# Kernel tuning notes

Measured on AMD Instinct MI355X. Metric: run time of the kernel, lower is better.

Reference implementation:

```python
import jax, jax.numpy as jnp
from jax import lax
import numpy as np

T, B = 64, 32          # timesteps, n_envs
C_IN, HW = 4, 64
H_LSTM = 256
FEAT = 64 * 4 * 4      # conv output flattened (1024)
FC = 512


def _conv(x, w, b, stride):
    # x: [N,C,H,W], w: [O,I,kh,kw] (torch OIHW), VALID padding like nn.Conv2d default
    y = lax.conv_general_dilated(x, w, (stride, stride), 'VALID',
                                 dimension_numbers=('NCHW', 'OIHW', 'NCHW'))
    return y + b[None, :, None, None]


def setup_inputs() -> dict:
    key = jax.random.key(0)
    ks = jax.random.split(key, 16)
    s = lambda *sh: sh
    d = {
        'x': jax.random.uniform(ks[0], (T * B, C_IN, HW, HW), jnp.float32) * 255.0,
        'done': jax.random.randint(ks[1], (T * B,), 0, 2, jnp.int32),
        'conv1_w': jax.random.normal(ks[2], (32, C_IN, 8, 8), jnp.float32) * 0.05,
        'conv1_b': jnp.zeros((32,), jnp.float32),
        'conv2_w': jax.random.normal(ks[3], (64, 32, 4, 4), jnp.float32) * 0.05,
        'conv2_b': jnp.zeros((64,), jnp.float32),
        'conv3_w': jax.random.normal(ks[4], (64, 64, 3, 3), jnp.float32) * 0.05,
        'conv3_b': jnp.zeros((64,), jnp.float32),
        'fc_w': jax.random.normal(ks[5], (FC, FEAT), jnp.float32) * 0.02,
        'fc_b': jnp.zeros((FC,), jnp.float32),
        'w_ih': jax.random.normal(ks[6], (4 * H_LSTM, FC), jnp.float32) * 0.03,
        'w_hh': jax.random.normal(ks[7], (4 * H_LSTM, H_LSTM), jnp.float32) * 0.03,
        'b_ih': jnp.zeros((4 * H_LSTM,), jnp.float32),
        'b_hh': jnp.zeros((4 * H_LSTM,), jnp.float32),
        'h0': jnp.zeros((1, B, H_LSTM), jnp.float32),
        'c0': jnp.zeros((1, B, H_LSTM), jnp.float32),
    }
    return d


def reference(x, done, conv1_w, conv1_b, conv2_w, conv2_b, conv3_w, conv3_b,
              fc_w, fc_b, w_ih, w_hh, b_ih, b_hh, h0, c0):
    # CNN encoder on x/255
    z = x / 255.0
    z = jax.nn.relu(_conv(z, conv1_w, conv1_b, 4))   # [TB,32,15,15]
    z = jax.nn.relu(_conv(z, conv2_w, conv2_b, 2))   # [TB,64,6,6]
    z = jax.nn.relu(_conv(z, conv3_w, conv3_b, 1))   # [TB,64,4,4]
    z = z.reshape(z.shape[0], -1)                    # [TB,1024]
    feats = jax.nn.relu(z @ fc_w.T + fc_b)           # [TB,512]

    n_envs = h0.shape[1]
    feats = feats.reshape(-1, n_envs, feats.shape[1])        # [T,B,512]
    mask = (1.0 - done.astype(feats.dtype)).reshape(-1, n_envs)  # [T,B]

    H = h0.shape[-1]

    def step(carry, inp):
        h, c = carry                    # [B,H] each
        f_t, m_t = inp                  # [B,512], [B]
        m = m_t[:, None]
        h = h * m
        c = c * m
        gates = f_t @ w_ih.T + b_ih + h @ w_hh.T + b_hh   # [B,4H]
        i, f, g, o = jnp.split(gates, 4, axis=-1)         # torch order: i,f,g,o
        c = jax.nn.sigmoid(f) * c + jax.nn.sigmoid(i) * jnp.tanh(g)
        h = jax.nn.sigmoid(o) * jnp.tanh(c)
        return (h, c), h

    (_, _), hs = lax.scan(step, (h0[0], c0[0]), (feats, mask))  # hs: [T,B,H]
    return hs.reshape(-1, H)   # [T*B, H]
```

## Files before the change

### kernel.cpp

```cpp
#include <hip/hip_runtime.h>
#include <math.h>


#define NIMG 2048

typedef _Float16 half2_t __attribute__((ext_vector_type(2)));
typedef __fp16 fp16x2_t __attribute__((ext_vector_type(2)));

__device__ inline unsigned short f2h_bits(float f) {
    union { _Float16 h; unsigned short u; } x;
    x.h = (_Float16)f;
    return x.u;
}

__device__ inline unsigned pack2_rne(float a, float b) {
    return (unsigned)f2h_bits(a) | ((unsigned)f2h_bits(b) << 16);
}

__device__ inline unsigned pack2_fast(float a, float b) {
#if __has_builtin(__builtin_amdgcn_cvt_pkrtz)
    union { fp16x2_t h; unsigned u; } x;
    x.h = __builtin_amdgcn_cvt_pkrtz(a, b);
    return x.u;
#else
    return pack2_rne(a, b);
#endif
}

__device__ inline float dot2(unsigned hu, unsigned wu, float acc) {
    union { unsigned u; half2_t h; } a, b;
    a.u = hu; b.u = wu;
#if __has_builtin(__builtin_amdgcn_fdot2)
    return __builtin_amdgcn_fdot2(a.h, b.h, acc, false);
#else
    return acc + (float)a.h.x * (float)b.h.x + (float)a.h.y * (float)b.h.y;
#endif
}

__device__ inline float fast_tanh(float x) {
    return 1.0f - 2.0f / (__expf(2.0f * x) + 1.0f);
}

__global__ void transpose_kernel(const float* __restrict__ in, float* __restrict__ out,
                                 int R, int C) {
    int idx = blockIdx.x * 256 + threadIdx.x;
    if (idx < R * C) {
        int r = idx / C, c = idx - r * C;
        out[c * R + r] = in[idx];
    }
}

__global__ void pack_whh_pairs_kernel(const float* __restrict__ whh,
                                      unsigned* __restrict__ wp) {
    int idx = blockIdx.x * 256 + threadIdx.x;
    if (idx >= 131072) return;
    int d4 = idx >> 12;
    int rem = idx & 4095;
    int row = rem >> 2;
    int j = idx & 3;
    int k0 = d4 * 8 + j * 2;
    const float* src = whh + (size_t)row * 256 + k0;
    wp[idx] = pack2_rne(src[0], src[1]);
}

__global__ void pack_w1_kernel(const float* __restrict__ w1, unsigned* __restrict__ w1p) {
    int idx = blockIdx.x * 256 + threadIdx.x;
    if (idx >= 4096) return;
    int oc = idx >> 7, rem = idx & 127;
    int ic = rem >> 5, ky = (rem >> 2) & 7, kxp = rem & 3;
    const float* src = w1 + (((size_t)oc * 4 + ic) * 8 + ky) * 8 + kxp * 2;
    w1p[idx] = pack2_rne(src[0], src[1]);
}

__global__ void pack_w2_kernel(const float* __restrict__ w2, unsigned* __restrict__ w2p) {
    int idx = blockIdx.x * 256 + threadIdx.x;
    if (idx >= 16384) return;
    int p = idx >> 6, oc = idx & 63;
    int ic = p >> 3, ky = (p >> 1) & 3, kxp = p & 1;
    const float* src = w2 + (size_t)oc * 512 + ic * 16 + ky * 4 + kxp * 2;
    w2p[idx] = pack2_rne(src[0], src[1]);
}

__global__ __launch_bounds__(1024) void conv1_kernel(const float* __restrict__ x,
                                                     const unsigned* __restrict__ w1p,
                                                     const float* __restrict__ b,
                                                     unsigned short* __restrict__ z1) {
    __shared__ unsigned short xs[4 * 64 * 64];
    int n = blockIdx.x;
    int tid = threadIdx.x;
    const float* xp = x + (size_t)n * 16384;
    const float inv = 1.0f / 255.0f;
    for (int i = tid * 4; i < 16384; i += 4096) {
        float4 v = *(const float4*)(xp + i);
        uint2 q;
        q.x = pack2_fast(v.x * inv, v.y * inv);
        q.y = pack2_fast(v.z * inv, v.w * inv);
        *(uint2*)&xs[i] = q;
    }
    __syncthreads();
    int lane = tid & 63, wave = tid >> 6;
    int gg = __builtin_amdgcn_readfirstlane(wave & 3);
    int pos = (wave >> 2) * 64 + lane;
    if (pos < 225) {
        int oy = pos / 15, ox = pos - oy * 15;
        float acc[8];
        const float* bp = b + gg * 8;
#pragma unroll
        for (int u = 0; u < 8; ++u) acc[u] = bp[u];
        for (int ic = 0; ic < 4; ++ic) {
#pragma unroll
            for (int ky = 0; ky < 8; ++ky) {
                const unsigned short* row = &xs[(ic * 64 + oy * 4 + ky) * 64 + ox * 4];
                uint2 qa = *(const uint2*)row;
                uint2 qb = *(const uint2*)(row + 4);
                const unsigned* wp = w1p + ((((gg * 8) * 4 + ic) * 8 + ky) * 4);
#pragma unroll
                for (int u = 0; u < 8; ++u) {
                    const unsigned* wu = wp + u * 128;
                    acc[u] = dot2(qa.x, wu[0], acc[u]);
                    acc[u] = dot2(qa.y, wu[1], acc[u]);
                    acc[u] = dot2(qb.x, wu[2], acc[u]);
                    acc[u] = dot2(qb.y, wu[3], acc[u]);
                }
            }
        }
        unsigned short* op = z1 + (size_t)n * 7680 + (gg * 8) * 240 + oy * 16 + ox;
#pragma unroll
        for (int u = 0; u < 8; ++u) op[u * 240] = f2h_bits(fmaxf(acc[u], 0.0f));
    }
}

__global__ __launch_bounds__(768) void conv2_kernel(const unsigned short* __restrict__ z1,
                                                    const unsigned* __restrict__ w2p,
                                                    const float* __restrict__ bias,
                                                    float* __restrict__ out) {
    __shared__ unsigned short xs[2][32 * 15 * 16];
    int tid = threadIdx.x;
    int n0 = blockIdx.x * 2;
#pragma unroll
    for (int img = 0; img < 2; ++img) {
        const unsigned* src = (const unsigned*)(z1 + (size_t)(n0 + img) * 7680);
        unsigned* dst = (unsigned*)xs[img];
        for (int i = tid; i < 3840; i += 768) dst[i] = src[i];
    }
    __syncthreads();
    int lane = tid & 63, wave = tid >> 6;
    int img = wave / 6;
    int oy = wave - img * 6;
    int n = n0 + img;
    float bv = bias[lane];
    float* op = out + (size_t)n * 2304 + lane * 36;
    float acc[6];
#pragma unroll
    for (int u = 0; u < 6; ++u) acc[u] = bv;
    for (int ic = 0; ic < 32; ++ic) {
#pragma unroll
        for (int ky = 0; ky < 4; ++ky) {
            const unsigned short* row = &xs[img][(ic * 15 + oy * 2 + ky) * 16];
            uint4 pa = *(const uint4*)row;
            uint4 pb = *(const uint4*)(row + 8);
            unsigned p[8] = {pa.x, pa.y, pa.z, pa.w, pb.x, pb.y, pb.z, pb.w};
            const unsigned* wpp = w2p + ((ic * 4 + ky) * 2) * 64 + lane;
            unsigned wa = wpp[0];
            unsigned wb = wpp[64];
#pragma unroll
            for (int u = 0; u < 6; ++u) {
                acc[u] = dot2(p[u], wa, acc[u]);
                acc[u] = dot2(p[u + 1], wb, acc[u]);
            }
        }
    }
#pragma unroll
    for (int u = 0; u < 6; ++u) op[oy * 6 + u] = fmaxf(acc[u], 0.0f);
}

__global__ __launch_bounds__(512) void conv3_kernel(const float* __restrict__ x,
                                                    const float* __restrict__ wt,
                                                    const float* __restrict__ bias,
                                                    float* __restrict__ out) {
    __shared__ float xs[4][64 * 6 * 8];
    int tid = threadIdx.x;
    int n0 = blockIdx.x * 4;
    for (int img = 0; img < 4; ++img) {
        const float* src = x + (size_t)(n0 + img) * 2304;
        for (int s = tid; s < 2304; s += 512) {
            int ic = s / 36;
            int rem = s - ic * 36;
            int r = rem / 6;
            int c = rem - r * 6;
            xs[img][(ic * 6 + r) * 8 + c] = src[s];
        }
    }
    __syncthreads();
    int lane = tid & 63, wave = tid >> 6;
    int img = wave >> 1;
    int half = wave & 1;
    int n = n0 + img;
    float bv = bias[lane];
    float* op = out + (size_t)n * 1024 + lane * 16;
    for (int q = 0; q < 2; ++q) {
        int oy = half * 2 + q;
        float acc[4];
#pragma unroll
        for (int u = 0; u < 4; ++u) acc[u] = bv;
        for (int ic = 0; ic < 64; ++ic) {
#pragma unroll
            for (int ky = 0; ky < 3; ++ky) {
                const float* xrow = &xs[img][(ic * 6 + oy + ky) * 8];
                float xr[8];
                *(float4*)&xr[0] = *(const float4*)&xrow[0];
                *(float4*)&xr[4] = *(const float4*)&xrow[4];
                const float* wp = wt + ((ic * 3 + ky) * 3) * 64 + lane;
#pragma unroll
                for (int kx = 0; kx < 3; ++kx) {
                    float wv = wp[kx * 64];
#pragma unroll
                    for (int u = 0; u < 4; ++u) acc[u] += xr[u + kx] * wv;
                }
            }
        }
#pragma unroll
        for (int u = 0; u < 4; ++u) op[oy * 4 + u] = fmaxf(acc[u], 0.0f);
    }
}

__global__ __launch_bounds__(256) void gemm_bt(const float* __restrict__ A,
                                               const float* __restrict__ B,
                                               const float* __restrict__ bias,
                                               const float* __restrict__ bias2,
                                               float* __restrict__ C,
                                               int M, int N, int K, int relu) {
    __shared__ float As[16][68];
    __shared__ float Bs[16][68];
    int tid = threadIdx.x;
    int m0 = blockIdx.y * 64, n0 = blockIdx.x * 64;
    int tx = tid & 15, ty = tid >> 4;
    int lr = tid >> 2;
    int lk = (tid & 3) * 4;
    const float* Ap = A + (size_t)(m0 + lr) * K + lk;
    const float* Bp = B + (size_t)(n0 + lr) * K + lk;
    float acc[4][4];
#pragma unroll
    for (int i = 0; i < 4; ++i)
#pragma unroll
        for (int j = 0; j < 4; ++j) acc[i][j] = 0.0f;

    for (int k0 = 0; k0 < K; k0 += 16) {
        float4 av = *(const float4*)(Ap + k0);
        float4 bv = *(const float4*)(Bp + k0);
        __syncthreads();
        As[lk + 0][lr] = av.x;
        As[lk + 1][lr] = av.y;
        As[lk + 2][lr] = av.z;
        As[lk + 3][lr] = av.w;
        Bs[lk + 0][lr] = bv.x;
        Bs[lk + 1][lr] = bv.y;
        Bs[lk + 2][lr] = bv.z;
        Bs[lk + 3][lr] = bv.w;
        __syncthreads();
#pragma unroll
        for (int kk = 0; kk < 16; ++kk) {
            float a[4], b[4];
            *(float4*)a = *(const float4*)&As[kk][ty * 4];
            *(float4*)b = *(const float4*)&Bs[kk][tx * 4];
#pragma unroll
            for (int i = 0; i < 4; ++i)
#pragma unroll
                for (int j = 0; j < 4; ++j) acc[i][j] += a[i] * b[j];
        }
    }
    float bb[4];
#pragma unroll
    for (int j = 0; j < 4; ++j) {
        float v = bias[n0 + tx * 4 + j];
        if (bias2) v += bias2[n0 + tx * 4 + j];
        bb[j] = v;
    }
#pragma unroll
    for (int i = 0; i < 4; ++i) {
        float4 o;
        o.x = acc[i][0] + bb[0];
        o.y = acc[i][1] + bb[1];
        o.z = acc[i][2] + bb[2];
        o.w = acc[i][3] + bb[3];
        if (relu) {
            o.x = fmaxf(o.x, 0.0f);
            o.y = fmaxf(o.y, 0.0f);
            o.z = fmaxf(o.z, 0.0f);
            o.w = fmaxf(o.w, 0.0f);
        }
        *(float4*)&C[(size_t)(m0 + ty * 4 + i) * N + n0 + tx * 4] = o;
    }
}

__global__ __launch_bounds__(1024) void lstm_kernel(const float* __restrict__ gi,
                                                    const unsigned* __restrict__ wp,
                                                    const int* __restrict__ done,
                                                    const float* __restrict__ h0,
                                                    const float* __restrict__ c0,
                                                    float* __restrict__ out) {
    __shared__ alignas(16) unsigned wo[32768];
    __shared__ alignas(16) unsigned h2u[128];
    __shared__ float xch[4096];
    int b = blockIdx.x, tt = threadIdx.x;
    int u = tt & 255, q = tt >> 8;
    int q8 = q * 8;

    const uint4* wsrc = (const uint4*)wp;

    {
        uint4* dst = (uint4*)wo;
        for (int i4 = tt; i4 < 8192; i4 += 1024) {
            int d4 = i4 >> 8, r = i4 & 255;
            dst[i4] = wsrc[d4 * 1024 + 768 + r];
        }
    }

#define LDW(j)                                              \
    uint4 wi##j = wsrc[(q8 + j) * 1024 + u];                \
    uint4 wf##j = wsrc[(q8 + j) * 1024 + 256 + u];          \
    uint4 wg##j = wsrc[(q8 + j) * 1024 + 512 + u];
    LDW(0) LDW(1) LDW(2) LDW(3) LDW(4) LDW(5) LDW(6) LDW(7)
#undef LDW

    if (tt < 128) {
        h2u[tt] = pack2_rne(h0[b * 256 + 2 * tt], h0[b * 256 + 2 * tt + 1]);
    }
    float c = 0.0f;
    float gv0 = 0.f, gv1 = 0.f, gv2 = 0.f, gv3 = 0.f;
    int dn = done[b];
    const float* gbase = gi + (size_t)b * 1024;
    if (q == 0) {
        c = c0[b * 256 + u];
        gv0 = gbase[u];
        gv1 = gbase[256 + u];
        gv2 = gbase[512 + u];
        gv3 = gbase[768 + u];
    }
    __syncthreads();

    const uint4* h2u4 = (const uint4*)h2u;
    const uint4* wo4 = (const uint4*)wo;

    for (int step = 0; step < 64; ++step) {
        int dnn = 0;
        if (step < 63) dnn = done[(step + 1) * 32 + b];
        float nx0 = 0.f, nx1 = 0.f, nx2 = 0.f, nx3 = 0.f;
        if (q == 0 && step < 63) {
            const float* gb = gbase + (size_t)(step + 1) * 32768;
            nx0 = gb[u];
            nx1 = gb[256 + u];
            nx2 = gb[512 + u];
            nx3 = gb[768 + u];
        }

        float pI = 0.f, pF = 0.f, pG = 0.f, pO = 0.f;
        if (!dn) {
#define MV(j) {                                                         \
        uint4 ha = h2u4[q8 + j];          \
        uint4 wv = wo4[(q8 + j) * 256 + u];   \
        pI = dot2(ha.x, wi##j.x, pI); pI = dot2(ha.y, wi##j.y, pI);     \
        pI = dot2(ha.z, wi##j.z, pI); pI = dot2(ha.w, wi##j.w, pI);     \
        pF = dot2(ha.x, wf##j.x, pF); pF = dot2(ha.y, wf##j.y, pF);     \
        pF = dot2(ha.z, wf##j.z, pF); pF = dot2(ha.w, wf##j.w, pF);     \
        pG = dot2(ha.x, wg##j.x, pG); pG = dot2(ha.y, wg##j.y, pG);     \
        pG = dot2(ha.z, wg##j.z, pG); pG = dot2(ha.w, wg##j.w, pG);     \
        pO = dot2(ha.x, wv.x, pO);    pO = dot2(ha.y, wv.y, pO);        \
        pO = dot2(ha.z, wv.z, pO);    pO = dot2(ha.w, wv.w, pO); }
            MV(0) MV(1) MV(2) MV(3) MV(4) MV(5) MV(6) MV(7)
#undef MV
        }

        xch[q * 1024 + u] = pI;
        xch[q * 1024 + 256 + u] = pF;
        xch[q * 1024 + 512 + u] = pG;
        xch[q * 1024 + 768 + u] = pO;
        __syncthreads();

        if (q == 0) {
            float m = 1.0f - (float)dn;
            float sI = xch[u] + xch[1024 + u] + xch[2048 + u] + xch[3072 + u];
            float sF = xch[256 + u] + xch[1280 + u] + xch[2304 + u] + xch[3328 + u];
            float sG = xch[512 + u] + xch[1536 + u] + xch[2560 + u] + xch[3584 + u];
            float sO = xch[768 + u] + xch[1792 + u] + xch[2816 + u] + xch[3840 + u];
            float g_i = gv0 + m * sI;
            float g_f = gv1 + m * sF;
            float g_g = gv2 + m * sG;
            float g_o = gv3 + m * sO;
            float si = 1.0f / (1.0f + __expf(-g_i));
            float sf = 1.0f / (1.0f + __expf(-g_f));
            float so = 1.0f / (1.0f + __expf(-g_o));
            float tg = fast_tanh(g_g);
            c = sf * (c * m) + si * tg;
            float hn = so * fast_tanh(c);
            out[((size_t)step * 32 + b) * 256 + u] = hn;
            float hn2 = __shfl_xor(hn, 1);
            if ((u & 1) == 0) {
                unsigned lo = f2h_bits(hn);
                unsigned hi = f2h_bits(hn2);
                h2u[u >> 1] = lo | (hi << 16);
            }
        }
        __syncthreads();

        gv0 = nx0; gv1 = nx1; gv2 = nx2; gv3 = nx3;
        dn = dnn;
    }
}

extern "C" void kernel_launch(void* const* d_in, const int* in_sizes, int n_in,
                              void* d_out, int out_size, void* d_ws, size_t ws_size,
                              hipStream_t stream) {
    const float* x    = (const float*)d_in[0];
    const int*   done = (const int*)d_in[1];
    const float* w1   = (const float*)d_in[2];
    const float* b1   = (const float*)d_in[3];
    const float* w2   = (const float*)d_in[4];
    const float* b2   = (const float*)d_in[5];
    const float* w3   = (const float*)d_in[6];
    const float* b3   = (const float*)d_in[7];
    const float* fcw  = (const float*)d_in[8];
    const float* fcb  = (const float*)d_in[9];
    const float* wih  = (const float*)d_in[10];
    const float* whh  = (const float*)d_in[11];
    const float* bih  = (const float*)d_in[12];
    const float* bhh  = (const float*)d_in[13];
    const float* h0   = (const float*)d_in[14];
    const float* c0   = (const float*)d_in[15];
    float* out = (float*)d_out;
    float* ws = (float*)d_ws;

    unsigned short* z1u = (unsigned short*)(ws + 0);
    float* z2    = ws + 8000000;
    float* z3    = ws + 0;
    float* feats = ws + 2097152;
    float* gi    = ws + 3145728;
    float* w3t   = ws + 13000000;
    unsigned* w1p = (unsigned*)(ws + 13100000);
    unsigned* w2p = (unsigned*)(ws + 13200000);
    unsigned* wp  = (unsigned*)(ws + 13300000);

    transpose_kernel<<<(64 * 576 + 255) / 256, 256, 0, stream>>>(w3, w3t, 64, 576);
    pack_whh_pairs_kernel<<<512, 256, 0, stream>>>(whh, wp);
    pack_w1_kernel<<<16, 256, 0, stream>>>(w1, w1p);
    pack_w2_kernel<<<64, 256, 0, stream>>>(w2, w2p);

    conv1_kernel<<<NIMG, 1024, 0, stream>>>(x, w1p, b1, z1u);
    conv2_kernel<<<NIMG / 2, 768, 0, stream>>>(z1u, w2p, b2, z2);
    conv3_kernel<<<NIMG / 4, 512, 0, stream>>>(z2, w3t, b3, z3);

    gemm_bt<<<dim3(512 / 64, NIMG / 64), 256, 0, stream>>>(z3, fcw, fcb, nullptr, feats,
                                                           NIMG, 512, 1024, 1);
    gemm_bt<<<dim3(1024 / 64, NIMG / 64), 256, 0, stream>>>(feats, wih, bih, bhh, gi,
                                                            NIMG, 1024, 512, 0);

    lstm_kernel<<<32, 1024, 0, stream>>>(gi, wp, done, h0, c0, out);
}
```

Before: 603.5 us.

## Run FC and input-gate GEMMs in packed fp16 with dot2 accumulation

conv3 now writes its output as packed fp16 pairs, and the fc and w_ih weights are packed to fp16 pairs at launch. A new GEMM uses dot2 instructions on those pairs with fp32 accumulation, and prefetches the next k-tile from global memory into registers while the current tile is computed. The aim is to halve GEMM operand traffic and the ALU ops per multiply-add. It also adds two packing kernels and extra fp16 rounding error on the features.

```diff
diff --git a/kernel.cpp b/kernel.cpp
--- a/kernel.cpp
+++ b/kernel.cpp
@@ -47,6 +47,15 @@
     if (idx < R * C) {
         int r = idx / C, c = idx - r * C;
         out[c * R + r] = in[idx];
+    }
+}
+
+__global__ void pack_pairs_kernel(const float* __restrict__ src,
+                                  unsigned* __restrict__ dst, int total) {
+    int idx = blockIdx.x * 256 + threadIdx.x;
+    if (idx < total) {
+        const float* s = src + (size_t)idx * 2;
+        dst[idx] = pack2_rne(s[0], s[1]);
     }
 }
 
@@ -177,7 +186,7 @@
 __global__ __launch_bounds__(512) void conv3_kernel(const float* __restrict__ x,
                                                     const float* __restrict__ wt,
                                                     const float* __restrict__ bias,
-                                                    float* __restrict__ out) {
+                                                    unsigned* __restrict__ outp) {
     __shared__ float xs[4][64 * 6 * 8];
     int tid = threadIdx.x;
     int n0 = blockIdx.x * 4;
@@ -197,7 +206,7 @@
     int half = wave & 1;
     int n = n0 + img;
     float bv = bias[lane];
-    float* op = out + (size_t)n * 1024 + lane * 16;
+    unsigned* op = outp + (size_t)n * 512 + lane * 8;
     for (int q = 0; q < 2; ++q) {
         int oy = half * 2 + q;
         float acc[4];
@@ -219,35 +228,38 @@
                 }
             }
         }
-#pragma unroll
-        for (int u = 0; u < 4; ++u) op[oy * 4 + u] = fmaxf(acc[u], 0.0f);
-    }
-}
-
-__global__ __launch_bounds__(256) void gemm_bt(const float* __restrict__ A,
-                                               const float* __restrict__ B,
-                                               const float* __restrict__ bias,
-                                               const float* __restrict__ bias2,
-                                               float* __restrict__ C,
-                                               int M, int N, int K, int relu) {
-    __shared__ float As[16][68];
-    __shared__ float Bs[16][68];
+        float a0 = fmaxf(acc[0], 0.0f), a1 = fmaxf(acc[1], 0.0f);
+        float a2 = fmaxf(acc[2], 0.0f), a3 = fmaxf(acc[3], 0.0f);
+        op[oy * 2 + 0] = pack2_rne(a0, a1);
+        op[oy * 2 + 1] = pack2_rne(a2, a3);
+    }
+}
+
+__global__ __launch_bounds__(256) void gemm_bt_h(const unsigned* __restrict__ A,
+                                                 const unsigned* __restrict__ B,
+                                                 const float* __restrict__ bias,
+                                                 const float* __restrict__ bias2,
+                                                 float* __restrict__ C,
+                                                 unsigned* __restrict__ Ch,
+                                                 int M, int N, int Kp, int relu) {
+    __shared__ unsigned As[16][66];
+    __shared__ unsigned Bs[16][66];
     int tid = threadIdx.x;
     int m0 = blockIdx.y * 64, n0 = blockIdx.x * 64;
     int tx = tid & 15, ty = tid >> 4;
     int lr = tid >> 2;
     int lk = (tid & 3) * 4;
-    const float* Ap = A + (size_t)(m0 + lr) * K + lk;
-    const float* Bp = B + (size_t)(n0 + lr) * K + lk;
+    const unsigned* Ap = A + (size_t)(m0 + lr) * Kp + lk;
+    const unsigned* Bp = B + (size_t)(n0 + lr) * Kp + lk;
     float acc[4][4];
 #pragma unroll
     for (int i = 0; i < 4; ++i)
 #pragma unroll
         for (int j = 0; j < 4; ++j) acc[i][j] = 0.0f;
 
-    for (int k0 = 0; k0 < K; k0 += 16) {
-        float4 av = *(const float4*)(Ap + k0);
-        float4 bv = *(const float4*)(Bp + k0);
+    uint4 av = *(const uint4*)Ap;
+    uint4 bv = *(const uint4*)Bp;
+    for (int k0 = 0; k0 < Kp; k0 += 16) {
         __syncthreads();
         As[lk + 0][lr] = av.x;
         As[lk + 1][lr] = av.y;
@@ -258,15 +270,19 @@
         Bs[lk + 2][lr] = bv.z;
         Bs[lk + 3][lr] = bv.w;
         __syncthreads();
+        if (k0 + 16 < Kp) {
+            av = *(const uint4*)(Ap + k0 + 16);
+            bv = *(const uint4*)(Bp + k0 + 16);
+        }
 #pragma unroll
         for (int kk = 0; kk < 16; ++kk) {
-            float a[4], b[4];
-            *(float4*)a = *(const float4*)&As[kk][ty * 4];
-            *(float4*)b = *(const float4*)&Bs[kk][tx * 4];
+            unsigned a[4], b[4];
+            *(uint4*)a = *(const uint4*)&As[kk][ty * 4];
+            *(uint4*)b = *(const uint4*)&Bs[kk][tx * 4];
 #pragma unroll
             for (int i = 0; i < 4; ++i)
 #pragma unroll
-                for (int j = 0; j < 4; ++j) acc[i][j] += a[i] * b[j];
+                for (int j = 0; j < 4; ++j) acc[i][j] = dot2(a[i], b[j], acc[i][j]);
         }
     }
     float bb[4];
@@ -289,7 +305,13 @@
             o.z = fmaxf(o.z, 0.0f);
             o.w = fmaxf(o.w, 0.0f);
         }
-        *(float4*)&C[(size_t)(m0 + ty * 4 + i) * N + n0 + tx * 4] = o;
+        size_t mrow = (size_t)(m0 + ty * 4 + i);
+        if (C) *(float4*)&C[mrow * N + n0 + tx * 4] = o;
+        if (Ch) {
+            unsigned* cp = Ch + mrow * (N >> 1) + (n0 >> 1) + tx * 2;
+            cp[0] = pack2_rne(o.x, o.y);
+            cp[1] = pack2_rne(o.z, o.w);
+        }
     }
 }
 
@@ -431,11 +453,13 @@
     float* ws = (float*)d_ws;
 
     unsigned short* z1u = (unsigned short*)(ws + 0);
-    float* z2    = ws + 8000000;
-    float* z3    = ws + 0;
-    float* feats = ws + 2097152;
-    float* gi    = ws + 3145728;
-    float* w3t   = ws + 13000000;
+    float* z2     = ws + 8000000;
+    unsigned* z3h = (unsigned*)(ws + 0);
+    unsigned* featsh = (unsigned*)(ws + 2097152);
+    float* gi     = ws + 3145728;
+    unsigned* fcwph = (unsigned*)(ws + 8000000);
+    unsigned* wihph = (unsigned*)(ws + 8300000);
+    float* w3t    = ws + 13000000;
     unsigned* w1p = (unsigned*)(ws + 13100000);
     unsigned* w2p = (unsigned*)(ws + 13200000);
     unsigned* wp  = (unsigned*)(ws + 13300000);
@@ -447,12 +471,15 @@
 
     conv1_kernel<<<NIMG, 1024, 0, stream>>>(x, w1p, b1, z1u);
     conv2_kernel<<<NIMG / 2, 768, 0, stream>>>(z1u, w2p, b2, z2);
-    conv3_kernel<<<NIMG / 4, 512, 0, stream>>>(z2, w3t, b3, z3);
-
-    gemm_bt<<<dim3(512 / 64, NIMG / 64), 256, 0, stream>>>(z3, fcw, fcb, nullptr, feats,
-                                                           NIMG, 512, 1024, 1);
-    gemm_bt<<<dim3(1024 / 64, NIMG / 64), 256, 0, stream>>>(feats, wih, bih, bhh, gi,
-                                                            NIMG, 1024, 512, 0);
+    conv3_kernel<<<NIMG / 4, 512, 0, stream>>>(z2, w3t, b3, z3h);
+
+    pack_pairs_kernel<<<(512 * 512 + 255) / 256, 256, 0, stream>>>(fcw, fcwph, 512 * 512);
+    pack_pairs_kernel<<<(1024 * 256 + 255) / 256, 256, 0, stream>>>(wih, wihph, 1024 * 256);
+
+    gemm_bt_h<<<dim3(512 / 64, NIMG / 64), 256, 0, stream>>>(
+        z3h, fcwph, fcb, nullptr, nullptr, featsh, NIMG, 512, 512, 1);
+    gemm_bt_h<<<dim3(1024 / 64, NIMG / 64), 256, 0, stream>>>(
+        featsh, wihph, bih, bhh, gi, nullptr, NIMG, 1024, 256, 0);
 
     lstm_kernel<<<32, 1024, 0, stream>>>(gi, wp, done, h0, c0, out);
 }
```

After: 566.0 us. 6.2% less time.
